# Performance work log

Measured on AMD Instinct MI355X. Metric: run time of the kernel, lower is better.

The kernel has to match this reference:

```python
import jax, jax.numpy as jnp
import numpy as np

N_NODES = 10000
N_EDGES = 160000
IN_DIM = 512
OUT_DIM = 512
ORDER = 2


def setup_inputs() -> dict:
    key = jax.random.key(0)
    ks = jax.random.split(key, 7)
    features = jax.random.normal(ks[0], (N_NODES, IN_DIM), dtype=jnp.float32)
    D_norm = jax.random.uniform(ks[1], (N_NODES, 1), dtype=jnp.float32)
    edge_w = jax.random.uniform(ks[2], (N_EDGES,), dtype=jnp.float32)
    # torch Linear weight is [out,in]; we store transposed [in,out] per hop
    W = jax.random.normal(ks[3], (ORDER + 1, IN_DIM, OUT_DIM), dtype=jnp.float32) * (1.0 / np.sqrt(IN_DIM))
    b = jax.random.normal(ks[4], (ORDER + 1, OUT_DIM), dtype=jnp.float32) * 0.01
    src = jax.random.randint(ks[5], (N_EDGES,), 0, N_NODES, dtype=jnp.int32)
    dst = jax.random.randint(ks[6], (N_EDGES,), 0, N_NODES, dtype=jnp.int32)
    return {"features": features, "D_norm": D_norm, "edge_w": edge_w,
            "W": W, "b": b, "src": src, "dst": dst}


def reference(features, D_norm, edge_w, W, b, src, dst):
    # GCNLayer.forward: dropout(p=0) is identity in eval; order SpMM hops
    n = features.shape[0]
    h_hop = [features]
    for _ in range(ORDER):
        # u_mul_e: gather src features, scale by edge weight, scatter-sum to dst
        msg = h_hop[-1][src] * edge_w[:, None]            # [E, in_dim]
        agg = jax.ops.segment_sum(msg, dst, num_segments=n)  # [N, in_dim]
        h_hop.append(agg * D_norm)                        # degree renorm
    # per-hop Linear + relu (batch_norm=False), then concat on feature dim
    h_part = [jax.nn.relu(h @ W[i] + b[i]) for i, h in enumerate(h_hop)]
    return jnp.concatenate(h_part, axis=1)               # [N, 3*out_dim]
```

## Files before the change

### kernel.cpp

```cpp
#include <hip/hip_runtime.h>
#include <hip/hip_bf16.h>


#define IN_DIM 512
#define OUT_DIM 512

typedef float f32x4 __attribute__((ext_vector_type(4)));
typedef unsigned short u16x8 __attribute__((ext_vector_type(8)));

__device__ inline unsigned short f2bf(float x) {
    union { float f; unsigned u; } v; v.f = x;
    unsigned r = v.u + 0x7fff + ((v.u >> 16) & 1);
    return (unsigned short)(r >> 16);
}
__device__ inline float bf2f(unsigned short h) {
    union { float f; unsigned u; } v; v.u = ((unsigned)h) << 16;
    return v.f;
}

__device__ inline void gld_lds16(const void* g, void* l) {
    __builtin_amdgcn_global_load_lds(
        (const __attribute__((address_space(1))) unsigned*)g,
        (__attribute__((address_space(3))) unsigned*)l, 16, 0, 0);
}

__device__ inline void mfma16(f32x4& d, u16x8 a, u16x8 b) {
    asm("v_mfma_f32_16x16x32_bf16 %0, %1, %2, %0" : "+v"(d) : "v"(a), "v"(b));
}


__global__ __launch_bounds__(256) void hist_kernel(const int* __restrict__ dst,
                                                   int* __restrict__ counts, int E) {
    int e = blockIdx.x * blockDim.x + threadIdx.x;
    if (e < E) atomicAdd(&counts[dst[e]], 1);
}

__global__ __launch_bounds__(1024) void scan_kernel(const int* __restrict__ counts,
                                                    int* __restrict__ offs,
                                                    int* __restrict__ cursor, int n) {
    __shared__ int partials[16];
    const int tid = threadIdx.x;
    const int chunk = (n + 1023) / 1024;
    const int start = tid * chunk;
    const int end = min(start + chunk, n);

    int sum = 0;
    for (int i = start; i < end; ++i) sum += counts[i];

    const int lane = tid & 63;
    const int wave = tid >> 6;
    int v = sum;
    #pragma unroll
    for (int d = 1; d < 64; d <<= 1) {
        int up = __shfl_up(v, d, 64);
        if (lane >= d) v += up;
    }
    if (lane == 63) partials[wave] = v;
    __syncthreads();
    if (tid == 0) {
        int acc = 0;
        #pragma unroll
        for (int w = 0; w < 16; ++w) { int t = partials[w]; partials[w] = acc; acc += t; }
    }
    __syncthreads();

    int run = partials[wave] + (v - sum);
    for (int i = start; i < end; ++i) {
        offs[i] = run;
        cursor[i] = run;
        run += counts[i];
    }
    if (end == n) offs[n] = run;
}

__global__ __launch_bounds__(256) void scatter_kernel(const int* __restrict__ src,
                                                      const int* __restrict__ dst,
                                                      const float* __restrict__ edge_w,
                                                      int* __restrict__ cursor,
                                                      int* __restrict__ esrc,
                                                      float* __restrict__ eww, int E) {
    int e = blockIdx.x * blockDim.x + threadIdx.x;
    if (e < E) {
        int d = dst[e];
        int pos = atomicAdd(&cursor[d], 1);
        esrc[pos] = src[e];
        eww[pos] = edge_w[e];
    }
}


__global__ __launch_bounds__(128) void hop_kernel(const float* __restrict__ hin,
                                                  const float* __restrict__ Dn,
                                                  const int* __restrict__ offs,
                                                  const int* __restrict__ esrc,
                                                  const float* __restrict__ eww,
                                                  float* __restrict__ hout) {
    const int v = blockIdx.x;
    const int t = threadIdx.x;
    const int beg = offs[v];
    const int end = offs[v + 1];
    float ax = 0.f, ay = 0.f, az = 0.f, aw = 0.f;
    int sN = 0; float wN = 0.f;
    if (beg < end) { sN = esrc[beg]; wN = eww[beg]; }
    for (int i = beg; i < end; ++i) {
        const int s = sN;
        const float w = wN;
        if (i + 1 < end) { sN = esrc[i + 1]; wN = eww[i + 1]; }
        const float4 x = *(const float4*)&hin[(size_t)s * IN_DIM + t * 4];
        ax = fmaf(x.x, w, ax);
        ay = fmaf(x.y, w, ay);
        az = fmaf(x.z, w, az);
        aw = fmaf(x.w, w, aw);
    }
    const float d = Dn[v];
    float4 r = {ax * d, ay * d, az * d, aw * d};
    *(float4*)&hout[(size_t)v * IN_DIM + t * 4] = r;
}


__global__ __launch_bounds__(256) void wsplit_kernel(const float* __restrict__ W,
                                                     unsigned short* __restrict__ WtHi,
                                                     unsigned short* __restrict__ WtLo) {
    const int t = blockIdx.x * 256 + threadIdx.x;
    const int kq = t & 127;
    const int n = (t >> 7) & 511;
    const int h = t >> 16;
    const float* w = W + (size_t)h * IN_DIM * OUT_DIM;
    unsigned short hi[4], lo[4];
    #pragma unroll
    for (int j = 0; j < 4; ++j) {
        const float x = w[(size_t)(kq * 4 + j) * OUT_DIM + n];
        hi[j] = f2bf(x);
        lo[j] = f2bf(x - bf2f(hi[j]));
    }
    const size_t o = (size_t)h * IN_DIM * OUT_DIM + (size_t)n * IN_DIM + kq * 4;
    *(ushort4*)&WtHi[o] = *(const ushort4*)hi;
    *(ushort4*)&WtLo[o] = *(const ushort4*)lo;
}


#define BM 128
#define BN 128
#define BK 32

__global__ __launch_bounds__(256) void gemm_split_mfma(
        const float* __restrict__ A0, const float* __restrict__ A1,
        const float* __restrict__ A2,
        const unsigned short* __restrict__ WtHi, const unsigned short* __restrict__ WtLo,
        const float* __restrict__ bias, float* __restrict__ out, int M) {

    __shared__ unsigned short Ahi[BM * BK];
    __shared__ unsigned short Alo[BM * BK];
    __shared__ unsigned short Bhi[BN * BK];
    __shared__ unsigned short Blo[BN * BK];

    const int tid = threadIdx.x;
    const int ln = tid & 63;
    const int wv = tid >> 6;
    const int hop = blockIdx.z;
    const float* __restrict__ A = hop == 0 ? A0 : hop == 1 ? A1 : A2;
    const unsigned short* __restrict__ BH = WtHi + (size_t)hop * IN_DIM * OUT_DIM;
    const unsigned short* __restrict__ BL = WtLo + (size_t)hop * IN_DIM * OUT_DIM;

    const int row0 = blockIdx.x * BM;
    const int col0 = blockIdx.y * BN;

    const int ar = tid >> 3;
    const int akq = tid & 7;
    const int bi = ln >> 2;
    const int bsl = ln & 3;

    const int wm = wv >> 1, wn = wv & 1;
    const int fr = ln & 15, kg = ln >> 4;

    f32x4 acc[4][4] = {};

    for (int kt = 0; kt < IN_DIM / BK; ++kt) {
        const int k0 = kt * BK;

        #pragma unroll
        for (int q = 0; q < 2; ++q) {
            const int nrow = (wv * 2 + q) * 16 + bi;
            const int kp = bsl ^ ((nrow >> 1) & 3);
            const size_t go = (size_t)(col0 + nrow) * IN_DIM + k0 + kp * 8;
            gld_lds16(BH + go, (char*)Bhi + (wv * 2 + q) * 1024);
            gld_lds16(BL + go, (char*)Blo + (wv * 2 + q) * 1024);
        }

        #pragma unroll
        for (int p = 0; p < 4; ++p) {
            const int r = ar + p * 32;
            int gr = row0 + r;
            gr = gr < M ? gr : M - 1;
            const float4 av = *(const float4*)&A[(size_t)gr * IN_DIM + k0 + akq * 4];
            unsigned short h[4], l[4];
            h[0] = f2bf(av.x); l[0] = f2bf(av.x - bf2f(h[0]));
            h[1] = f2bf(av.y); l[1] = f2bf(av.y - bf2f(h[1]));
            h[2] = f2bf(av.z); l[2] = f2bf(av.z - bf2f(h[2]));
            h[3] = f2bf(av.w); l[3] = f2bf(av.w - bf2f(h[3]));
            const int boff = r * 64 + ((akq * 8) ^ ((((r >> 1) & 3)) << 4));
            *(ushort4*)((char*)Ahi + boff) = *(const ushort4*)h;
            *(ushort4*)((char*)Alo + boff) = *(const ushort4*)l;
        }

        __syncthreads();

        u16x8 ah[4], al[4], bh[4], bl[4];
        #pragma unroll
        for (int mf = 0; mf < 4; ++mf) {
            const int r = wm * 64 + mf * 16 + fr;
            const int off = r * 64 + ((kg * 16) ^ ((((r >> 1) & 3)) << 4));
            ah[mf] = *(const u16x8*)((const char*)Ahi + off);
            al[mf] = *(const u16x8*)((const char*)Alo + off);
        }
        #pragma unroll
        for (int nf = 0; nf < 4; ++nf) {
            const int n = wn * 64 + nf * 16 + fr;
            const int off = n * 64 + ((kg * 16) ^ ((((n >> 1) & 3)) << 4));
            bh[nf] = *(const u16x8*)((const char*)Bhi + off);
            bl[nf] = *(const u16x8*)((const char*)Blo + off);
        }

        #pragma unroll
        for (int mf = 0; mf < 4; ++mf)
            #pragma unroll
            for (int nf = 0; nf < 4; ++nf)
                mfma16(acc[mf][nf], al[mf], bh[nf]);
        #pragma unroll
        for (int mf = 0; mf < 4; ++mf)
            #pragma unroll
            for (int nf = 0; nf < 4; ++nf)
                mfma16(acc[mf][nf], ah[mf], bl[nf]);
        #pragma unroll
        for (int mf = 0; mf < 4; ++mf)
            #pragma unroll
            for (int nf = 0; nf < 4; ++nf)
                mfma16(acc[mf][nf], ah[mf], bh[nf]);

        __syncthreads();
    }

    asm volatile("s_nop 7\n\ts_nop 7" ::: );

    const int rb = row0 + wm * 64;
    const int cb = col0 + wn * 64;
    #pragma unroll
    for (int nf = 0; nf < 4; ++nf) {
        const int c = cb + nf * 16 + fr;
        const float bv = bias[hop * OUT_DIM + c];
        #pragma unroll
        for (int mf = 0; mf < 4; ++mf) {
            #pragma unroll
            for (int j = 0; j < 4; ++j) {
                const int r = rb + mf * 16 + kg * 4 + j;
                if (r < M) {
                    float v = acc[mf][nf][j] + bv;
                    out[(size_t)r * (3 * OUT_DIM) + hop * OUT_DIM + c] = v > 0.f ? v : 0.f;
                }
            }
        }
    }
}


extern "C" void kernel_launch(void* const* d_in, const int* in_sizes, int n_in,
                              void* d_out, int out_size, void* d_ws, size_t ws_size,
                              hipStream_t stream) {
    const float* features = (const float*)d_in[0];
    const float* D_norm   = (const float*)d_in[1];
    const float* edge_w   = (const float*)d_in[2];
    const float* W        = (const float*)d_in[3];
    const float* b        = (const float*)d_in[4];
    const int*   src      = (const int*)d_in[5];
    const int*   dst      = (const int*)d_in[6];
    const int N = in_sizes[1];
    const int E = in_sizes[2];
    float* out = (float*)d_out;

    char* w = (char*)d_ws;
    auto alloc = [&](size_t bytes) {
        void* p = (void*)w;
        w += (bytes + 255) & ~(size_t)255;
        return p;
    };
    int*            counts = (int*)alloc((size_t)N * 4);
    int*            offs   = (int*)alloc((size_t)(N + 1) * 4);
    int*            cursor = (int*)alloc((size_t)N * 4);
    int*            esrc   = (int*)alloc((size_t)E * 4);
    float*          eww    = (float*)alloc((size_t)E * 4);
    float*          h1     = (float*)alloc((size_t)N * IN_DIM * 4);
    float*          h2     = (float*)alloc((size_t)N * IN_DIM * 4);
    unsigned short* wthi   = (unsigned short*)alloc((size_t)3 * IN_DIM * OUT_DIM * 2);
    unsigned short* wtlo   = (unsigned short*)alloc((size_t)3 * IN_DIM * OUT_DIM * 2);

    hipMemsetAsync(counts, 0, (size_t)N * 4, stream);
    hist_kernel<<<(E + 255) / 256, 256, 0, stream>>>(dst, counts, E);
    scan_kernel<<<1, 1024, 0, stream>>>(counts, offs, cursor, N);
    scatter_kernel<<<(E + 255) / 256, 256, 0, stream>>>(src, dst, edge_w, cursor, esrc, eww, E);

    wsplit_kernel<<<(3 * IN_DIM * (OUT_DIM / 4)) / 256, 256, 0, stream>>>(W, wthi, wtlo);

    hop_kernel<<<N, 128, 0, stream>>>(features, D_norm, offs, esrc, eww, h1);
    hop_kernel<<<N, 128, 0, stream>>>(h1, D_norm, offs, esrc, eww, h2);

    dim3 grid((N + BM - 1) / BM, OUT_DIM / BN, 3);
    gemm_split_mfma<<<grid, 256, 0, stream>>>(features, h1, h2, wthi, wtlo, b, out, N);
}
```

Before: 290.6 us.

## Double-buffer GEMM LDS tiles and split hop SpMM into feature slices

The GEMM now keeps two LDS buffers. It prefetches the next K-tile of B by direct global-to-LDS loads and of A into registers while MFMAs run on the current tile, which removes one barrier per iteration and overlaps memory latency with compute. The hop SpMM is restructured so each wave handles one node over a 64-float feature slice, with 8 slice blocks per group of 4 nodes. This gives more parallel blocks and keeps each slice's working set cache-friendly. The costs are doubled LDS use, which may lower occupancy, and scalar rather than float4 gathers plus extra index reloads in the hop kernel.

```diff
diff --git a/kernel.cpp b/kernel.cpp
--- a/kernel.cpp
+++ b/kernel.cpp
@@ -89,32 +89,31 @@
 }
 
 
-__global__ __launch_bounds__(128) void hop_kernel(const float* __restrict__ hin,
-                                                  const float* __restrict__ Dn,
-                                                  const int* __restrict__ offs,
-                                                  const int* __restrict__ esrc,
-                                                  const float* __restrict__ eww,
-                                                  float* __restrict__ hout) {
-    const int v = blockIdx.x;
-    const int t = threadIdx.x;
+__global__ __launch_bounds__(256) void hop_slice_kernel(const float* __restrict__ hin,
+                                                        const float* __restrict__ Dn,
+                                                        const int* __restrict__ offs,
+                                                        const int* __restrict__ esrc,
+                                                        const float* __restrict__ eww,
+                                                        float* __restrict__ hout, int N) {
+    const int bid = blockIdx.x;
+    const int slice = bid & 7;
+    const int wv = threadIdx.x >> 6;
+    const int v = (bid >> 3) * 4 + wv;
+    if (v >= N) return;
+    const int f = slice * 64 + (threadIdx.x & 63);
+
     const int beg = offs[v];
     const int end = offs[v + 1];
-    float ax = 0.f, ay = 0.f, az = 0.f, aw = 0.f;
+    float acc = 0.f;
     int sN = 0; float wN = 0.f;
     if (beg < end) { sN = esrc[beg]; wN = eww[beg]; }
     for (int i = beg; i < end; ++i) {
         const int s = sN;
         const float w = wN;
         if (i + 1 < end) { sN = esrc[i + 1]; wN = eww[i + 1]; }
-        const float4 x = *(const float4*)&hin[(size_t)s * IN_DIM + t * 4];
-        ax = fmaf(x.x, w, ax);
-        ay = fmaf(x.y, w, ay);
-        az = fmaf(x.z, w, az);
-        aw = fmaf(x.w, w, aw);
-    }
-    const float d = Dn[v];
-    float4 r = {ax * d, ay * d, az * d, aw * d};
-    *(float4*)&hout[(size_t)v * IN_DIM + t * 4] = r;
+        acc = fmaf(hin[(size_t)s * IN_DIM + f], w, acc);
+    }
+    hout[(size_t)v * IN_DIM + f] = acc * Dn[v];
 }
 
 
@@ -142,6 +141,7 @@
 #define BM 128
 #define BN 128
 #define BK 32
+#define NT (IN_DIM / BK)
 
 __global__ __launch_bounds__(256) void gemm_split_mfma(
         const float* __restrict__ A0, const float* __restrict__ A1,
@@ -149,10 +149,7 @@
         const unsigned short* __restrict__ WtHi, const unsigned short* __restrict__ WtLo,
         const float* __restrict__ bias, float* __restrict__ out, int M) {
 
-    __shared__ unsigned short Ahi[BM * BK];
-    __shared__ unsigned short Alo[BM * BK];
-    __shared__ unsigned short Bhi[BN * BK];
-    __shared__ unsigned short Blo[BN * BK];
+    __shared__ unsigned short lds[2][4][BM * BK];
 
     const int tid = threadIdx.x;
     const int ln = tid & 63;
@@ -173,52 +170,74 @@
     const int wm = wv >> 1, wn = wv & 1;
     const int fr = ln & 15, kg = ln >> 4;
 
-    f32x4 acc[4][4] = {};
-
-    for (int kt = 0; kt < IN_DIM / BK; ++kt) {
-        const int k0 = kt * BK;
-
+    auto stageB = [&](int b, int k0) {
         #pragma unroll
         for (int q = 0; q < 2; ++q) {
             const int nrow = (wv * 2 + q) * 16 + bi;
             const int kp = bsl ^ ((nrow >> 1) & 3);
             const size_t go = (size_t)(col0 + nrow) * IN_DIM + k0 + kp * 8;
-            gld_lds16(BH + go, (char*)Bhi + (wv * 2 + q) * 1024);
-            gld_lds16(BL + go, (char*)Blo + (wv * 2 + q) * 1024);
-        }
-
+            gld_lds16(BH + go, (char*)lds[b][2] + (wv * 2 + q) * 1024);
+            gld_lds16(BL + go, (char*)lds[b][3] + (wv * 2 + q) * 1024);
+        }
+    };
+    auto loadA = [&](float4* apf, int k0) {
+        #pragma unroll
+        for (int p = 0; p < 4; ++p) {
+            int gr = row0 + ar + p * 32;
+            gr = gr < M ? gr : M - 1;
+            apf[p] = *(const float4*)&A[(size_t)gr * IN_DIM + k0 + akq * 4];
+        }
+    };
+    auto writeA = [&](int b, const float4* apf) {
         #pragma unroll
         for (int p = 0; p < 4; ++p) {
             const int r = ar + p * 32;
-            int gr = row0 + r;
-            gr = gr < M ? gr : M - 1;
-            const float4 av = *(const float4*)&A[(size_t)gr * IN_DIM + k0 + akq * 4];
+            const float4 av = apf[p];
             unsigned short h[4], l[4];
             h[0] = f2bf(av.x); l[0] = f2bf(av.x - bf2f(h[0]));
             h[1] = f2bf(av.y); l[1] = f2bf(av.y - bf2f(h[1]));
             h[2] = f2bf(av.z); l[2] = f2bf(av.z - bf2f(h[2]));
             h[3] = f2bf(av.w); l[3] = f2bf(av.w - bf2f(h[3]));
             const int boff = r * 64 + ((akq * 8) ^ ((((r >> 1) & 3)) << 4));
-            *(ushort4*)((char*)Ahi + boff) = *(const ushort4*)h;
-            *(ushort4*)((char*)Alo + boff) = *(const ushort4*)l;
-        }
-
-        __syncthreads();
+            *(ushort4*)((char*)lds[b][0] + boff) = *(const ushort4*)h;
+            *(ushort4*)((char*)lds[b][1] + boff) = *(const ushort4*)l;
+        }
+    };
+
+    f32x4 acc[4][4] = {};
+
+    {
+        stageB(0, 0);
+        float4 apf[4];
+        loadA(apf, 0);
+        writeA(0, apf);
+    }
+    __syncthreads();
+
+    #pragma unroll 1
+    for (int t = 0; t < NT; ++t) {
+        const int cur = t & 1;
+
+        float4 apf[4];
+        if (t + 1 < NT) {
+            stageB(cur ^ 1, (t + 1) * BK);
+            loadA(apf, (t + 1) * BK);
+        }
 
         u16x8 ah[4], al[4], bh[4], bl[4];
         #pragma unroll
         for (int mf = 0; mf < 4; ++mf) {
             const int r = wm * 64 + mf * 16 + fr;
             const int off = r * 64 + ((kg * 16) ^ ((((r >> 1) & 3)) << 4));
-            ah[mf] = *(const u16x8*)((const char*)Ahi + off);
-            al[mf] = *(const u16x8*)((const char*)Alo + off);
+            ah[mf] = *(const u16x8*)((const char*)lds[cur][0] + off);
+            al[mf] = *(const u16x8*)((const char*)lds[cur][1] + off);
         }
         #pragma unroll
         for (int nf = 0; nf < 4; ++nf) {
             const int n = wn * 64 + nf * 16 + fr;
             const int off = n * 64 + ((kg * 16) ^ ((((n >> 1) & 3)) << 4));
-            bh[nf] = *(const u16x8*)((const char*)Bhi + off);
-            bl[nf] = *(const u16x8*)((const char*)Blo + off);
+            bh[nf] = *(const u16x8*)((const char*)lds[cur][2] + off);
+            bl[nf] = *(const u16x8*)((const char*)lds[cur][3] + off);
         }
 
         #pragma unroll
@@ -236,6 +255,8 @@
             #pragma unroll
             for (int nf = 0; nf < 4; ++nf)
                 mfma16(acc[mf][nf], ah[mf], bh[nf]);
+
+        if (t + 1 < NT) writeA(cur ^ 1, apf);
 
         __syncthreads();
     }
@@ -300,8 +321,9 @@
 
     wsplit_kernel<<<(3 * IN_DIM * (OUT_DIM / 4)) / 256, 256, 0, stream>>>(W, wthi, wtlo);
 
-    hop_kernel<<<N, 128, 0, stream>>>(features, D_norm, offs, esrc, eww, h1);
-    hop_kernel<<<N, 128, 0, stream>>>(h1, D_norm, offs, esrc, eww, h2);
+    const int hop_blocks = ((N + 3) / 4) * 8;
+    hop_slice_kernel<<<hop_blocks, 256, 0, stream>>>(features, D_norm, offs, esrc, eww, h1, N);
+    hop_slice_kernel<<<hop_blocks, 256, 0, stream>>>(h1, D_norm, offs, esrc, eww, h2, N);
 
     dim3 grid((N + BM - 1) / BM, OUT_DIM / BN, 3);
     gemm_split_mfma<<<grid, 256, 0, stream>>>(features, h1, h2, wthi, wtlo, b, out, N);
```

After: 313.9 us. +8.0%, slower.
